# Performance work log

Measured on AMD Instinct MI355X. Metric: run time of the kernel, lower is better.

## Reference

```python
import jax, jax.numpy as jnp
import numpy as np

L, D, FF, H, S, B, W = 4, 768, 3072, 12, 4096, 4, 128


def setup_inputs() -> dict:
    key = jax.random.key(0)
    ks = jax.random.split(key, 8)
    w_ = lambda k, shape: jax.random.normal(k, shape, jnp.float32) * 0.02
    return {
        "x": jax.random.normal(ks[0], (B, S, D), jnp.float32),
        "Wq": w_(ks[1], (L, D, D)), "bq": jnp.zeros((L, D), jnp.float32),
        "Wk": w_(ks[2], (L, D, D)), "bk": jnp.zeros((L, D), jnp.float32),
        "Wv": w_(ks[3], (L, D, D)), "bv": jnp.zeros((L, D), jnp.float32),
        "W1": w_(ks[4], (L, D, FF)), "b1": jnp.zeros((L, FF), jnp.float32),
        "W2": w_(ks[5], (L, FF, D)), "b2": jnp.zeros((L, D), jnp.float32),
        "g1": jnp.ones((L, D), jnp.float32), "beta1": jnp.zeros((L, D), jnp.float32),
        "g2": jnp.ones((L, D), jnp.float32), "beta2": jnp.zeros((L, D), jnp.float32),
        "n_heads": H,
        "window": W,
    }


def _layernorm(x, g, b, eps=1e-5):
    m = jnp.mean(x, axis=-1, keepdims=True)
    v = jnp.mean(jnp.square(x - m), axis=-1, keepdims=True)
    return (x - m) * jax.lax.rsqrt(v + eps) * g + b


def _sliding_attn(x, Wq, bq, Wk, bk, Wv, bv, n_heads, w):
    # Longformer 'sliding_chunks' self-attention, one-sided window w (band 2w+1).
    b_, s_, d_ = x.shape
    hd = d_ // n_heads
    nc = s_ // w  # number of query chunks of size w

    def proj(Wm, bm):
        p = x @ Wm + bm
        return p.reshape(b_, s_, n_heads, hd).transpose(0, 2, 1, 3)  # [B,H,S,hd]

    q = proj(Wq, bq) / jnp.sqrt(jnp.asarray(hd, x.dtype))
    k = proj(Wk, bk)
    v = proj(Wv, bv)

    # pad keys/values by one window each side so every query chunk sees 3w keys
    kp = jnp.pad(k, ((0, 0), (0, 0), (w, w), (0, 0)))
    vp = jnp.pad(v, ((0, 0), (0, 0), (w, w), (0, 0)))
    idx = jnp.arange(nc)[:, None] * w + jnp.arange(3 * w)[None, :]  # [nc, 3w]
    kb = kp[:, :, idx]  # [B,H,nc,3w,hd]
    vb = vp[:, :, idx]
    qc = q.reshape(b_, n_heads, nc, w, hd)

    scores = jnp.einsum('bhcqd,bhckd->bhcqk', qc, kb)  # [B,H,nc,w,3w]

    # band + boundary mask: key pos = c*w + kj - w, query pos = c*w + qi
    c = jnp.arange(nc)[:, None, None]
    qi = jnp.arange(w)[None, :, None]
    kj = jnp.arange(3 * w)[None, None, :]
    rel = kj - qi - w
    kpos = c * w + kj - w
    mask = (jnp.abs(rel) <= w) & (kpos >= 0) & (kpos < s_)  # [nc,w,3w]

    scores = jnp.where(mask[None, None], scores, -jnp.inf)
    attn = jax.nn.softmax(scores, axis=-1)
    out = jnp.einsum('bhcqk,bhckd->bhcqd', attn, vb)  # [B,H,nc,w,hd]
    return out.reshape(b_, n_heads, s_, hd).transpose(0, 2, 1, 3).reshape(b_, s_, d_)


def reference(x, Wq, bq, Wk, bk, Wv, bv, W1, b1, W2, b2, g1, beta1, g2, beta2,
              n_heads, window):
    n_layers = Wq.shape[0]
    for l in range(n_layers):
        attn = _sliding_attn(x, Wq[l], bq[l], Wk[l], bk[l], Wv[l], bv[l],
                             n_heads, window)
        x = _layernorm(x + attn, g1[l], beta1[l])
        h = jnp.maximum(x @ W1[l] + b1[l], 0.0) @ W2[l] + b2[l]
        x = _layernorm(x + h, g2[l], beta2[l])
    return x
```

## Files before the change

kernel.cpp:

```cpp
#include <hip/hip_runtime.h>
#include <hip/hip_bf16.h>
#include <type_traits>

#define LAYERS 4
#define D      768
#define FF     3072
#define NH     12
#define HD     64
#define SEQ    4096
#define BATCH  4
#define WIN    128
#define NC     (SEQ / WIN)
#define NTOK   (BATCH * SEQ)

using bf16 = __hip_bfloat16;
typedef short short8 __attribute__((ext_vector_type(8)));
typedef short short4v __attribute__((ext_vector_type(4)));
typedef float floatx4 __attribute__((ext_vector_type(4)));

__device__ __forceinline__ float b2f(unsigned short u) {
    return __uint_as_float(((unsigned)u) << 16);
}
__device__ __forceinline__ short f2bs(float f) {
    union { bf16 h; short s; } u; u.h = __float2bfloat16(f); return u.s;
}
__device__ __forceinline__ void st_cvt(float* p, float v) { *p = v; }
__device__ __forceinline__ void st_cvt(bf16* p, float v) { *p = __float2bfloat16(v); }

__device__ __forceinline__ void gl_lds16(const void* g, void* l) {
    __builtin_amdgcn_global_load_lds(
        (const __attribute__((address_space(1))) void*)g,
        (__attribute__((address_space(3))) void*)l, 16, 0, 0);
}

#define SB0   __builtin_amdgcn_sched_barrier(0)
#define BAR   __builtin_amdgcn_s_barrier()
#define VM4   asm volatile("s_waitcnt vmcnt(4)" ::: "memory")
#define VM0   asm volatile("s_waitcnt vmcnt(0)" ::: "memory")
#define SP1   __builtin_amdgcn_s_setprio(1)
#define SP0   __builtin_amdgcn_s_setprio(0)

__global__ __launch_bounds__(256)
void cvt_f32_bf16(const float* __restrict__ src, bf16* __restrict__ dst)
{
    const int i = (blockIdx.x * 256 + threadIdx.x) * 8;
    const float4 a0 = *(const float4*)(src + i);
    const float4 a1 = *(const float4*)(src + i + 4);
    short8 p = { f2bs(a0.x), f2bs(a0.y), f2bs(a0.z), f2bs(a0.w),
                 f2bs(a1.x), f2bs(a1.y), f2bs(a1.z), f2bs(a1.w) };
    *(short8*)((short*)dst + i) = p;
}

__global__ __launch_bounds__(256)
void transpose_cvt(const float* __restrict__ src, bf16* __restrict__ dst, int K, int N)
{
    __shared__ float t[32][33];
    const int n0 = blockIdx.x * 32, k0 = blockIdx.y * 32;
    const int tx = threadIdx.x & 31, ty = threadIdx.x >> 5;
    #pragma unroll
    for (int r = 0; r < 4; ++r)
        t[ty + 8 * r][tx] = src[(size_t)(k0 + ty + 8 * r) * N + n0 + tx];
    __syncthreads();
    #pragma unroll
    for (int r = 0; r < 4; ++r)
        dst[(size_t)(n0 + ty + 8 * r) * K + k0 + tx] = __float2bfloat16(t[tx][ty + 8 * r]);
}

template<int OMODE, int RELU>
__global__ __launch_bounds__(512, 2)
void gemm8(const bf16* __restrict__ A, const bf16* __restrict__ Wt,
           const float* __restrict__ b0, const float* __restrict__ b1p,
           const float* __restrict__ b2p, bf16* __restrict__ C,
           int K, int N)
{
    extern __shared__ char ldsc[];
    const int tid  = threadIdx.x;
    const int lane = tid & 63;
    const int wave = tid >> 6;
    const int quad = lane >> 4, l16 = lane & 15;
    const int wm = wave >> 2, wn = wave & 3;

    const int bx  = blockIdx.x;
    const int bxs = (bx & 7) * 8 + (bx >> 3);
    const int row0 = bxs * 256;
    const int col0 = blockIdx.y * 256;

    const int lin0 = wave * 1024 + lane * 16;
    const int lin1 = 8192 + wave * 1024 + lane * 16;
    const int rl0 = lin0 >> 7, rl1 = lin1 >> 7;
    const int so0 = (lin0 & 127) ^ ((rl0 & 7) << 4);
    const int so1 = (lin1 & 127) ^ ((rl1 & 7) << 4);
    const char* agl0 = (const char*)A  + 2 * ((size_t)(row0 + rl0) * K) + so0;
    const char* agl1 = (const char*)A  + 2 * ((size_t)(row0 + rl1) * K) + so1;
    const char* bgl0 = (const char*)Wt + 2 * ((size_t)(col0 + rl0) * K) + so0;
    const char* bgl1 = (const char*)Wt + 2 * ((size_t)(col0 + rl1) * K) + so1;
    const size_t hstr = (size_t)128 * K * 2;

#define STA(d,h,kt) do { \
    gl_lds16(agl0 + ((h) ? hstr : 0) + (size_t)(kt) * 128, ldsc + ((d)*2+(h))*16384 + lin0); \
    gl_lds16(agl1 + ((h) ? hstr : 0) + (size_t)(kt) * 128, ldsc + ((d)*2+(h))*16384 + lin1); } while (0)
#define STB(d,h,kt) do { \
    gl_lds16(bgl0 + ((h) ? hstr : 0) + (size_t)(kt) * 128, ldsc + 65536 + ((d)*2+(h))*16384 + lin0); \
    gl_lds16(bgl1 + ((h) ? hstr : 0) + (size_t)(kt) * 128, ldsc + 65536 + ((d)*2+(h))*16384 + lin1); } while (0)

    const int arow  = wm * 64 + l16;
    const int abase = arow * 128;
    const int sA    = (arow & 7) << 4;
    const int aof0  = (quad * 16) ^ sA;
    const int aof1  = (64 + quad * 16) ^ sA;
    const int brow  = wn * 32 + l16;
    const int bbase = brow * 128;
    const int sB    = (brow & 7) << 4;
    const int bof0  = (quad * 16) ^ sB;
    const int bof1  = (64 + quad * 16) ^ sB;

    short8 af[4][2], bf0[2][2], bf1[2][2];
    floatx4 acc[2][2][4][2];
    const floatx4 zero = {0.f, 0.f, 0.f, 0.f};
    #pragma unroll
    for (int a = 0; a < 2; ++a)
        #pragma unroll
        for (int b = 0; b < 2; ++b)
            #pragma unroll
            for (int m = 0; m < 4; ++m)
                #pragma unroll
                for (int n = 0; n < 2; ++n) acc[a][b][m][n] = zero;

#define LDA(slot) do { const char* ab_ = ldsc + (slot)*16384 + abase; \
    _Pragma("unroll") for (int m_ = 0; m_ < 4; ++m_) { \
        af[m_][0] = *(const short8*)(ab_ + m_*2048 + aof0); \
        af[m_][1] = *(const short8*)(ab_ + m_*2048 + aof1); } } while (0)
#define LDB(slot, BF) do { const char* bb_ = ldsc + 65536 + (slot)*16384 + bbase; \
    _Pragma("unroll") for (int n_ = 0; n_ < 2; ++n_) { \
        BF[n_][0] = *(const short8*)(bb_ + n_*2048 + bof0); \
        BF[n_][1] = *(const short8*)(bb_ + n_*2048 + bof1); } } while (0)
#define MM(mh, nh, BF) do { \
    _Pragma("unroll") for (int m_ = 0; m_ < 4; ++m_) \
    _Pragma("unroll") for (int n_ = 0; n_ < 2; ++n_) { \
        acc[mh][nh][m_][n_] = __builtin_amdgcn_mfma_f32_16x16x32_bf16(af[m_][0], BF[n_][0], acc[mh][nh][m_][n_], 0, 0, 0); \
        acc[mh][nh][m_][n_] = __builtin_amdgcn_mfma_f32_16x16x32_bf16(af[m_][1], BF[n_][1], acc[mh][nh][m_][n_], 0, 0, 0); } } while (0)

    const int nkt   = K >> 6;
    const int niter = K >> 7;

    STA(0,0,0); STB(0,0,0); STA(0,1,0); STB(0,1,0);
    STA(1,0,1); STB(1,0,1);
    VM4; SB0; BAR; SB0;

    for (int i = 0; i < niter; ++i) {
        const int k1 = 2*i + 1;
        const int k2 = (2*i + 2 < nkt) ? 2*i + 2 : nkt - 1;
        const int k3 = (2*i + 3 < nkt) ? 2*i + 3 : nkt - 1;
        LDA(0); LDB(0, bf0); LDB(1, bf1); STA(1,1,k1); STB(1,1,k1);
        SP1; MM(0,0,bf0); MM(0,1,bf1); SP0; SB0; BAR; SB0;
        LDA(1); STA(0,0,k2); STB(0,0,k2);
        SP1; MM(1,0,bf0); MM(1,1,bf1); SP0; VM4; SB0; BAR; SB0;
        LDA(2); LDB(2, bf0); LDB(3, bf1); STA(0,1,k2); STB(0,1,k2);
        SP1; MM(0,0,bf0); MM(0,1,bf1); SP0; SB0; BAR; SB0;
        LDA(3); STA(1,0,k3); STB(1,0,k3);
        SP1; MM(1,0,bf0); MM(1,1,bf1); SP0; VM4; SB0; BAR; SB0;
    }
    VM0;

#undef STA
#undef STB
#undef LDA
#undef LDB
#undef MM

    constexpr size_t QEc = (size_t)BATCH * NH * SEQ * HD;
    int sel = 0;
    const float* bptr = b0;
    float scl = 1.0f;
    int ccb = col0;
    if constexpr (OMODE == 3) {
        sel  = blockIdx.y / 3;
        bptr = (sel == 0) ? b0 : (sel == 1) ? b1p : b2p;
        scl  = (sel == 0) ? 0.125f : 1.0f;
        ccb  = col0 - sel * 768;
    }
    #pragma unroll
    for (int mh = 0; mh < 2; ++mh)
    #pragma unroll
    for (int nh = 0; nh < 2; ++nh)
    #pragma unroll
    for (int n = 0; n < 2; ++n) {
        const int c  = ccb + nh * 128 + wn * 32 + n * 16 + l16;
        const float bvv = bptr[c];
        #pragma unroll
        for (int m = 0; m < 4; ++m) {
            const int rr0 = row0 + mh * 128 + wm * 64 + m * 16 + quad * 4;
            if constexpr (OMODE == 3) {
                if (sel == 2) {
                    short4v pack;
                    #pragma unroll
                    for (int r = 0; r < 4; ++r)
                        pack[r] = f2bs(acc[mh][nh][m][n][r] + bvv);
                    const int b_ = rr0 >> 12, s_ = rr0 & (SEQ - 1);
                    const int h_ = c >> 6, d_ = c & (HD - 1);
                    bf16* Cv = C + 2 * QEc;
                    *(short4v*)&Cv[(((size_t)(b_ * NH + h_)) * HD + d_) * SEQ + s_] = pack;
                } else {
                    bf16* Cq = C + (size_t)sel * QEc;
                    #pragma unroll
                    for (int r = 0; r < 4; ++r) {
                        const float v = (acc[mh][nh][m][n][r] + bvv) * scl;
                        const int rr = rr0 + r;
                        const int b_ = rr >> 12, s_ = rr & (SEQ - 1);
                        const int h_ = c >> 6, d_ = c & (HD - 1);
                        Cq[(((size_t)(b_ * NH + h_)) * SEQ + s_) * HD + d_] = __float2bfloat16(v);
                    }
                }
            } else {
                #pragma unroll
                for (int r = 0; r < 4; ++r) {
                    float v = acc[mh][nh][m][n][r] + bvv;
                    if (RELU) v = fmaxf(v, 0.f);
                    C[(size_t)(rr0 + r) * N + c] = __float2bfloat16(v);
                }
            }
        }
    }
}

template<int RELU, int OMODE>
__global__ __launch_bounds__(256)
void mfma_gemm_bf(const bf16* __restrict__ A, const bf16* __restrict__ Wt,
                  const float* __restrict__ bias, bf16* __restrict__ C,
                  int M, int N, int K, float scale)
{
    __shared__ __align__(16) short As[128 * 32];
    __shared__ __align__(16) short Bs[128 * 32];
    const int tid  = threadIdx.x;
    const int lane = tid & 63;
    const int wave = tid >> 6;
    const int quad = lane >> 4, l16 = lane & 15;
    const int mw = (wave >> 1) * 64, nw = (wave & 1) * 64;
    const int row0 = blockIdx.x * 128;
    const int col0 = blockIdx.y * 128;

    const unsigned short* Ag = (const unsigned short*)A;
    const unsigned short* Bg = (const unsigned short*)Wt;
    const int sr = lane >> 2;
    const int sc = (lane & 3) * 8;

    floatx4 acc[4][4];
    const floatx4 zero = {0.f, 0.f, 0.f, 0.f};
    #pragma unroll
    for (int i = 0; i < 4; ++i)
        #pragma unroll
        for (int j = 0; j < 4; ++j) acc[i][j] = zero;

    const size_t abase = (size_t)row0 * K;
    const size_t bbase = (size_t)col0 * K;

    for (int k0 = 0; k0 < K; k0 += 32) {
        __syncthreads();
        #pragma unroll
        for (int e = 0; e < 2; ++e) {
            const int seg = wave * 2 + e;
            const int r = seg * 16 + sr;
            gl_lds16(Ag + abase + (size_t)r * K + k0 + sc, &As[seg * 512]);
            gl_lds16(Bg + bbase + (size_t)r * K + k0 + sc, &Bs[seg * 512]);
        }
        __syncthreads();
        short8 af[4], bfr[4];
        #pragma unroll
        for (int i = 0; i < 4; ++i)
            af[i] = *(const short8*)&As[(mw + 16 * i + l16) * 32 + quad * 8];
        #pragma unroll
        for (int j = 0; j < 4; ++j)
            bfr[j] = *(const short8*)&Bs[(nw + 16 * j + l16) * 32 + quad * 8];
        #pragma unroll
        for (int i = 0; i < 4; ++i)
            #pragma unroll
            for (int j = 0; j < 4; ++j)
                acc[i][j] = __builtin_amdgcn_mfma_f32_16x16x32_bf16(af[i], bfr[j], acc[i][j], 0, 0, 0);
    }
    #pragma unroll
    for (int j = 0; j < 4; ++j) {
        const int c = col0 + nw + 16 * j + l16;
        const float bv = bias[c];
        #pragma unroll
        for (int i = 0; i < 4; ++i) {
            const int rr0 = row0 + mw + 16 * i + quad * 4;
            if constexpr (OMODE == 2) {
                short4v pack;
                #pragma unroll
                for (int r = 0; r < 4; ++r)
                    pack[r] = f2bs((acc[i][j][r] + bv) * scale);
                const int b_ = rr0 >> 12, s_ = rr0 & (SEQ - 1);
                const int h_ = c >> 6, d_ = c & (HD - 1);
                *(short4v*)&C[(((size_t)(b_ * NH + h_)) * HD + d_) * SEQ + s_] = pack;
            } else {
                #pragma unroll
                for (int r = 0; r < 4; ++r) {
                    float v = acc[i][j][r] + bv;
                    if (RELU) v = fmaxf(v, 0.f);
                    v *= scale;
                    const int rr = rr0 + r;
                    if constexpr (OMODE == 1) {
                        const int b_ = rr >> 12, s_ = rr & (SEQ - 1);
                        const int h_ = c >> 6, d_ = c & (HD - 1);
                        st_cvt(&C[(((size_t)(b_ * NH + h_)) * SEQ + s_) * HD + d_], v);
                    } else {
                        st_cvt(&C[(size_t)rr * N + c], v);
                    }
                }
            }
        }
    }
}

__global__ __launch_bounds__(256, 2)
void attn_mfma_kernel(const bf16* __restrict__ q, const bf16* __restrict__ k,
                      const bf16* __restrict__ v, bf16* __restrict__ out)
{
    __shared__ __align__(16) short Qs[128][72];
    __shared__ __align__(16) short Ks[64][72];
    __shared__ __align__(16) short Vs[64][72];
    __shared__ __align__(16) short Ps[4][32][72];

    const int c = blockIdx.x, h = blockIdx.y, b = blockIdx.z;
    const int tid = threadIdx.x;
    const int wave = tid >> 6, lane = tid & 63;
    const int quad = lane >> 4, l16 = lane & 15;
    const int qbase = wave * 32;

    const unsigned short* qg = (const unsigned short*)q + ((size_t)(b * NH + h)) * SEQ * HD;
    const unsigned short* kg = (const unsigned short*)k + ((size_t)(b * NH + h)) * SEQ * HD;
    const unsigned short* vg = (const unsigned short*)v + ((size_t)(b * NH + h)) * HD * SEQ;

    #pragma unroll
    for (int e = 0; e < 4; ++e) {
        const int idx = tid + e * 256;
        const int row = idx >> 3, d0 = (idx & 7) * 8;
        *(uint4*)&Qs[row][d0] = *(const uint4*)(qg + (size_t)(c * WIN + row) * HD + d0);
    }

    floatx4 O[2][4];
    const floatx4 zero = {0.f, 0.f, 0.f, 0.f};
    float m_i[2][4], l_i[2][4];
    #pragma unroll
    for (int i = 0; i < 2; ++i)
        #pragma unroll
        for (int r = 0; r < 4; ++r) { m_i[i][r] = -1e30f; l_i[i][r] = 0.f; }
    #pragma unroll
    for (int i = 0; i < 2; ++i)
        #pragma unroll
        for (int dj = 0; dj < 4; ++dj) O[i][dj] = zero;

    for (int sl = 0; sl < 6; ++sl) {
        const int s0 = sl * 64;
        const int kpos0 = c * WIN - WIN + s0;
        if (kpos0 < 0 || kpos0 >= SEQ) continue;
        __syncthreads();
        #pragma unroll
        for (int e = 0; e < 2; ++e) {
            const int idx = tid + e * 256;
            const int row = idx >> 3, d0 = (idx & 7) * 8;
            *(uint4*)&Ks[row][d0] = *(const uint4*)(kg + (size_t)(kpos0 + row) * HD + d0);
            *(uint4*)&Vs[row][d0] = *(const uint4*)(vg + (size_t)row * SEQ + kpos0 + d0);
        }
        __syncthreads();
        short8 aq[2][2], bk2[4][2];
        #pragma unroll
        for (int i = 0; i < 2; ++i)
            #pragma unroll
            for (int hh = 0; hh < 2; ++hh)
                aq[i][hh] = *(const short8*)&Qs[qbase + 16 * i + l16][hh * 32 + quad * 8];
        #pragma unroll
        for (int j = 0; j < 4; ++j)
            #pragma unroll
            for (int hh = 0; hh < 2; ++hh)
                bk2[j][hh] = *(const short8*)&Ks[16 * j + l16][hh * 32 + quad * 8];
        floatx4 sc[2][4];
        #pragma unroll
        for (int i = 0; i < 2; ++i)
            #pragma unroll
            for (int j = 0; j < 4; ++j) {
                floatx4 t = __builtin_amdgcn_mfma_f32_16x16x32_bf16(aq[i][0], bk2[j][0], zero, 0, 0, 0);
                sc[i][j]  = __builtin_amdgcn_mfma_f32_16x16x32_bf16(aq[i][1], bk2[j][1], t, 0, 0, 0);
            }
        #pragma unroll
        for (int i = 0; i < 2; ++i) {
            #pragma unroll
            for (int r = 0; r < 4; ++r) {
                const int qq = qbase + 16 * i + quad * 4 + r;
                float sv[4];
                float mx = -1e30f;
                #pragma unroll
                for (int j = 0; j < 4; ++j) {
                    const int kj = s0 + 16 * j + l16;
                    const bool ok = (kj >= qq) && (kj <= qq + 2 * WIN);
                    const float s = ok ? sc[i][j][r] : -1e30f;
                    sv[j] = s;
                    mx = fmaxf(mx, s);
                }
                mx = fmaxf(mx, __shfl_xor(mx, 1));
                mx = fmaxf(mx, __shfl_xor(mx, 2));
                mx = fmaxf(mx, __shfl_xor(mx, 4));
                mx = fmaxf(mx, __shfl_xor(mx, 8));
                const float mn = fmaxf(m_i[i][r], mx);
                const float corr = __expf(m_i[i][r] - mn);
                m_i[i][r] = mn;
                float ps = 0.f;
                #pragma unroll
                for (int j = 0; j < 4; ++j) {
                    const float p = (sv[j] > -0.9e30f) ? __expf(sv[j] - mn) : 0.f;
                    ps += p;
                    Ps[wave][16 * i + quad * 4 + r][16 * j + l16] = f2bs(p);
                }
                ps += __shfl_xor(ps, 1);
                ps += __shfl_xor(ps, 2);
                ps += __shfl_xor(ps, 4);
                ps += __shfl_xor(ps, 8);
                l_i[i][r] = l_i[i][r] * corr + ps;
                #pragma unroll
                for (int dj = 0; dj < 4; ++dj) O[i][dj][r] *= corr;
            }
        }
        short8 ap[2][2], bv2[4][2];
        #pragma unroll
        for (int i = 0; i < 2; ++i)
            #pragma unroll
            for (int hh = 0; hh < 2; ++hh)
                ap[i][hh] = *(const short8*)&Ps[wave][16 * i + l16][hh * 32 + quad * 8];
        #pragma unroll
        for (int dj = 0; dj < 4; ++dj)
            #pragma unroll
            for (int hh = 0; hh < 2; ++hh)
                bv2[dj][hh] = *(const short8*)&Vs[16 * dj + l16][hh * 32 + quad * 8];
        #pragma unroll
        for (int i = 0; i < 2; ++i)
            #pragma unroll
            for (int dj = 0; dj < 4; ++dj) {
                O[i][dj] = __builtin_amdgcn_mfma_f32_16x16x32_bf16(ap[i][0], bv2[dj][0], O[i][dj], 0, 0, 0);
                O[i][dj] = __builtin_amdgcn_mfma_f32_16x16x32_bf16(ap[i][1], bv2[dj][1], O[i][dj], 0, 0, 0);
            }
    }
    bf16* og = out + ((size_t)b * SEQ + c * WIN) * D + h * HD;
    #pragma unroll
    for (int i = 0; i < 2; ++i) {
        #pragma unroll
        for (int r = 0; r < 4; ++r) {
            const float inv = 1.f / l_i[i][r];
            const int qq = qbase + 16 * i + quad * 4 + r;
            #pragma unroll
            for (int dj = 0; dj < 4; ++dj)
                og[(size_t)qq * D + 16 * dj + l16] = __float2bfloat16(O[i][dj][r] * inv);
        }
    }
}

template<int WBF>
__global__ __launch_bounds__(256)
void add_ln_kernel(const float* __restrict__ xin, const bf16* __restrict__ h,
                   float* __restrict__ xout, bf16* __restrict__ xbf,
                   const float* __restrict__ g, const float* __restrict__ beta)
{
    const int row  = blockIdx.x * 4 + (threadIdx.x >> 6);
    const int lane = threadIdx.x & 63;
    const float* xr = xin + (size_t)row * D;
    const unsigned short* hr = (const unsigned short*)h + (size_t)row * D;
    float t[12];
    float s = 0.f, s2 = 0.f;
    #pragma unroll
    for (int e = 0; e < 3; ++e) {
        const int i = lane * 4 + e * 256;
        const float4  xv = *(const float4*)(xr + i);
        const short4v hv = *(const short4v*)(hr + i);
        #pragma unroll
        for (int j = 0; j < 4; ++j) {
            const float tv = ((const float*)&xv)[j] + b2f(((const unsigned short*)&hv)[j]);
            t[e * 4 + j] = tv; s += tv; s2 += tv * tv;
        }
    }
    #pragma unroll
    for (int off = 1; off < 64; off <<= 1) {
        s  += __shfl_xor(s, off);
        s2 += __shfl_xor(s2, off);
    }
    const float mean = s * (1.f / D);
    const float inv  = rsqrtf(s2 * (1.f / D) - mean * mean + 1e-5f);
    #pragma unroll
    for (int e = 0; e < 3; ++e) {
        const int i = lane * 4 + e * 256;
        const float4 gv = *(const float4*)(g + i);
        const float4 bv = *(const float4*)(beta + i);
        float4 ov; short4v pb;
        #pragma unroll
        for (int j = 0; j < 4; ++j) {
            const float val = (t[e * 4 + j] - mean) * inv * ((const float*)&gv)[j]
                              + ((const float*)&bv)[j];
            ((float*)&ov)[j] = val;
            pb[j] = f2bs(val);
        }
        *(float4*)(xout + (size_t)row * D + i) = ov;
        if constexpr (WBF)
            *(short4v*)((short*)xbf + (size_t)row * D + i) = pb;
    }
}

static void transpose_layer(const float* Wq, const float* Wk, const float* Wv,
                            const float* W1, const float* W2, int l,
                            bf16* wtl, hipStream_t stream)
{
    const size_t DDm = (size_t)D * D, DFFm = (size_t)D * FF;
    transpose_cvt<<<dim3(D / 32, D / 32), 256, 0, stream>>>(
        Wq + (size_t)l * DDm, wtl, D, D);
    transpose_cvt<<<dim3(D / 32, D / 32), 256, 0, stream>>>(
        Wk + (size_t)l * DDm, wtl + DDm, D, D);
    transpose_cvt<<<dim3(D / 32, D / 32), 256, 0, stream>>>(
        Wv + (size_t)l * DDm, wtl + 2 * DDm, D, D);
    transpose_cvt<<<dim3(FF / 32, D / 32), 256, 0, stream>>>(
        W1 + (size_t)l * DFFm, wtl + 3 * DDm, D, FF);
    transpose_cvt<<<dim3(D / 32, FF / 32), 256, 0, stream>>>(
        W2 + (size_t)l * DFFm, wtl + 3 * DDm + DFFm, FF, D);
}

static void run_fast8(const float* x0,
                      const float* Wq, const float* bq, const float* Wk, const float* bk,
                      const float* Wv, const float* bv, const float* W1, const float* b1,
                      const float* W2, const float* b2, const float* g1, const float* be1,
                      const float* g2, const float* be2, float* out,
                      bf16* qb, bf16* kb, bf16* vb, bf16* hb, bf16* mid, bf16* h2,
                      bf16* wt, bf16* xbf, bool hoisted, hipStream_t stream)
{
    const dim3 gQKV(64, 9);
    const dim3 gF1(64, 12);
    const dim3 gF2(64, 3);
    const dim3 ga(NC, NH, BATCH);
    const size_t DDm = (size_t)D * D, DFFm = (size_t)D * FF;
    const size_t LW = 3 * DDm + 2 * DFFm;
    const int SMEM = 131072;

    cvt_f32_bf16<<<NTOK * D / 2048, 256, 0, stream>>>(x0, xbf);
    if (hoisted)
        for (int l = 0; l < LAYERS; ++l)
            transpose_layer(Wq, Wk, Wv, W1, W2, l, wt + (size_t)l * LW, stream);

    for (int l = 0; l < LAYERS; ++l) {
        const float* xin = (l == 0) ? x0 : out;
        bf16* wtl = hoisted ? wt + (size_t)l * LW : wt;
        if (!hoisted)
            transpose_layer(Wq, Wk, Wv, W1, W2, l, wtl, stream);

        gemm8<3, 0><<<gQKV, 512, SMEM, stream>>>(
            xbf, wtl, bq + (size_t)l * D, bk + (size_t)l * D, bv + (size_t)l * D,
            qb, D, 2304);
        attn_mfma_kernel<<<ga, 256, 0, stream>>>(qb, kb, vb, hb);
        add_ln_kernel<1><<<NTOK / 4, 256, 0, stream>>>(xin, hb, out, xbf,
            g1 + (size_t)l * D, be1 + (size_t)l * D);
        gemm8<0, 1><<<gF1, 512, SMEM, stream>>>(
            xbf, wtl + 3 * DDm, b1 + (size_t)l * FF, nullptr, nullptr,
            mid, D, FF);
        gemm8<0, 0><<<gF2, 512, SMEM, stream>>>(
            mid, wtl + 3 * DDm + DFFm, b2 + (size_t)l * D, nullptr, nullptr,
            h2, FF, D);
        add_ln_kernel<1><<<NTOK / 4, 256, 0, stream>>>(out, h2, out, xbf,
            g2 + (size_t)l * D, be2 + (size_t)l * D);
    }
}

static void run_fast_old(const float* x0,
                         const float* Wq, const float* bq, const float* Wk, const float* bk,
                         const float* Wv, const float* bv, const float* W1, const float* b1,
                         const float* W2, const float* b2, const float* g1, const float* be1,
                         const float* g2, const float* be2, float* out,
                         bf16* qb, bf16* kb, bf16* vb, bf16* hb, bf16* mid, bf16* h2,
                         bf16* wt, bf16* xbf, hipStream_t stream)
{
    const dim3 gD(NTOK / 128, D / 128);
    const dim3 gF(NTOK / 128, FF / 128);
    const dim3 ga(NC, NH, BATCH);
    const size_t DDm = (size_t)D * D, DFFm = (size_t)D * FF;

    cvt_f32_bf16<<<NTOK * D / 2048, 256, 0, stream>>>(x0, xbf);
    for (int l = 0; l < LAYERS; ++l) {
        const float* xin = (l == 0) ? x0 : out;
        transpose_layer(Wq, Wk, Wv, W1, W2, l, wt, stream);

        mfma_gemm_bf<0, 1><<<gD, 256, 0, stream>>>(
            xbf, wt, bq + (size_t)l * D, qb, NTOK, D, D, 0.125f);
        mfma_gemm_bf<0, 1><<<gD, 256, 0, stream>>>(
            xbf, wt + DDm, bk + (size_t)l * D, kb, NTOK, D, D, 1.0f);
        mfma_gemm_bf<0, 2><<<gD, 256, 0, stream>>>(
            xbf, wt + 2 * DDm, bv + (size_t)l * D, vb, NTOK, D, D, 1.0f);
        attn_mfma_kernel<<<ga, 256, 0, stream>>>(qb, kb, vb, hb);
        add_ln_kernel<1><<<NTOK / 4, 256, 0, stream>>>(xin, hb, out, xbf,
            g1 + (size_t)l * D, be1 + (size_t)l * D);
        mfma_gemm_bf<1, 0><<<gF, 256, 0, stream>>>(
            xbf, wt + 3 * DDm, b1 + (size_t)l * FF, mid, NTOK, FF, D, 1.0f);
        mfma_gemm_bf<0, 0><<<gD, 256, 0, stream>>>(
            mid, wt + 3 * DDm + DFFm, b2 + (size_t)l * D, h2, NTOK, D, FF, 1.0f);
        add_ln_kernel<1><<<NTOK / 4, 256, 0, stream>>>(out, h2, out, xbf,
            g2 + (size_t)l * D, be2 + (size_t)l * D);
    }
}

extern "C" void kernel_launch(void* const* d_in, const int* in_sizes, int n_in,
                              void* d_out, int out_size, void* d_ws, size_t ws_size,
                              hipStream_t stream)
{
    const float* x0  = (const float*)d_in[0];
    const float* Wq  = (const float*)d_in[1];
    const float* bq  = (const float*)d_in[2];
    const float* Wk  = (const float*)d_in[3];
    const float* bk  = (const float*)d_in[4];
    const float* Wv  = (const float*)d_in[5];
    const float* bv  = (const float*)d_in[6];
    const float* W1  = (const float*)d_in[7];
    const float* b1  = (const float*)d_in[8];
    const float* W2  = (const float*)d_in[9];
    const float* b2  = (const float*)d_in[10];
    const float* g1  = (const float*)d_in[11];
    const float* be1 = (const float*)d_in[12];
    const float* g2  = (const float*)d_in[13];
    const float* be2 = (const float*)d_in[14];
    float* out = (float*)d_out;

    const size_t QE = (size_t)BATCH * NH * SEQ * HD;
    const size_t LW = (size_t)3 * D * D + 2 * (size_t)D * FF;
    bf16* qb  = (bf16*)d_ws;
    bf16* kb  = qb + QE;
    bf16* vb  = kb + QE;
    bf16* hb  = vb + QE;
    bf16* mid = qb;
    bf16* h2  = qb + 4 * QE;
    bf16* wt  = qb + 5 * QE;
    const bool tierA = ws_size >= (6 * QE + (size_t)LAYERS * LW) * sizeof(bf16);
    const bool tierB = ws_size >= (6 * QE + LW) * sizeof(bf16);
    bf16* xbf = wt + (tierA ? (size_t)LAYERS * LW : LW);

    static int attr_state = 0;
    if (attr_state == 0) {
        bool ok = true;
        ok &= hipFuncSetAttribute((const void*)(gemm8<3, 0>),
              hipFuncAttributeMaxDynamicSharedMemorySize, 131072) == hipSuccess;
        ok &= hipFuncSetAttribute((const void*)(gemm8<0, 1>),
              hipFuncAttributeMaxDynamicSharedMemorySize, 131072) == hipSuccess;
        ok &= hipFuncSetAttribute((const void*)(gemm8<0, 0>),
              hipFuncAttributeMaxDynamicSharedMemorySize, 131072) == hipSuccess;
        attr_state = ok ? 1 : -1;
    }

    if (tierB && attr_state == 1) {
        run_fast8(x0, Wq, bq, Wk, bk, Wv, bv, W1, b1, W2, b2, g1, be1, g2, be2,
                  out, qb, kb, vb, hb, mid, h2, wt, xbf, tierA, stream);
    } else if (tierB) {
        run_fast_old(x0, Wq, bq, Wk, bk, Wv, bv, W1, b1, W2, b2, g1, be1, g2, be2,
                     out, qb, kb, vb, hb, mid, h2, wt, xbf, stream);
    }
}
```

Baseline: 1.612 ms.

## Replace 256x256 GEMM with smaller 128x256 tile, static LDS, double buffering

Swaps the large 256x256-tile GEMM, which used 128 KB of dynamic LDS and a four-stage interleaved schedule, for a 128x256 tile with a K-step of 32 and a simple two-buffer pipeline in 48 KB of static LDS. Launch bounds move to 4 blocks per CU and the row grid doubles. The aim is more resident blocks and better latency hiding without the dynamic-LDS attribute setup. In exchange each tile reuses operands less, and every K-step pays a full vmcnt(0) wait plus a barrier. The fallback path now also runs when the workspace is too small.

```diff
diff --git a/kernel.cpp b/kernel.cpp
--- a/kernel.cpp
+++ b/kernel.cpp
@@ -35,7 +35,6 @@
 
 #define SB0   __builtin_amdgcn_sched_barrier(0)
 #define BAR   __builtin_amdgcn_s_barrier()
-#define VM4   asm volatile("s_waitcnt vmcnt(4)" ::: "memory")
 #define VM0   asm volatile("s_waitcnt vmcnt(0)" ::: "memory")
 #define SP1   __builtin_amdgcn_s_setprio(1)
 #define SP0   __builtin_amdgcn_s_setprio(0)
@@ -67,13 +66,13 @@
 }
 
 template<int OMODE, int RELU>
-__global__ __launch_bounds__(512, 2)
-void gemm8(const bf16* __restrict__ A, const bf16* __restrict__ Wt,
+__global__ __launch_bounds__(512, 4)
+void gemm2(const bf16* __restrict__ A, const bf16* __restrict__ Wt,
            const float* __restrict__ b0, const float* __restrict__ b1p,
            const float* __restrict__ b2p, bf16* __restrict__ C,
            int K, int N)
 {
-    extern __shared__ char ldsc[];
+    __shared__ __align__(16) char lds[49152];
     const int tid  = threadIdx.x;
     const int lane = tid & 63;
     const int wave = tid >> 6;
@@ -81,92 +80,70 @@
     const int wm = wave >> 2, wn = wave & 3;
 
     const int bx  = blockIdx.x;
-    const int bxs = (bx & 7) * 8 + (bx >> 3);
-    const int row0 = bxs * 256;
+    const int bxs = (bx & 7) * 16 + (bx >> 3);
+    const int row0 = bxs * 128;
     const int col0 = blockIdx.y * 256;
 
-    const int lin0 = wave * 1024 + lane * 16;
-    const int lin1 = 8192 + wave * 1024 + lane * 16;
-    const int rl0 = lin0 >> 7, rl1 = lin1 >> 7;
-    const int so0 = (lin0 & 127) ^ ((rl0 & 7) << 4);
-    const int so1 = (lin1 & 127) ^ ((rl1 & 7) << 4);
-    const char* agl0 = (const char*)A  + 2 * ((size_t)(row0 + rl0) * K) + so0;
-    const char* agl1 = (const char*)A  + 2 * ((size_t)(row0 + rl1) * K) + so1;
-    const char* bgl0 = (const char*)Wt + 2 * ((size_t)(col0 + rl0) * K) + so0;
-    const char* bgl1 = (const char*)Wt + 2 * ((size_t)(col0 + rl1) * K) + so1;
-    const size_t hstr = (size_t)128 * K * 2;
-
-#define STA(d,h,kt) do { \
-    gl_lds16(agl0 + ((h) ? hstr : 0) + (size_t)(kt) * 128, ldsc + ((d)*2+(h))*16384 + lin0); \
-    gl_lds16(agl1 + ((h) ? hstr : 0) + (size_t)(kt) * 128, ldsc + ((d)*2+(h))*16384 + lin1); } while (0)
-#define STB(d,h,kt) do { \
-    gl_lds16(bgl0 + ((h) ? hstr : 0) + (size_t)(kt) * 128, ldsc + 65536 + ((d)*2+(h))*16384 + lin0); \
-    gl_lds16(bgl1 + ((h) ? hstr : 0) + (size_t)(kt) * 128, ldsc + 65536 + ((d)*2+(h))*16384 + lin1); } while (0)
-
-    const int arow  = wm * 64 + l16;
-    const int abase = arow * 128;
-    const int sA    = (arow & 7) << 4;
-    const int aof0  = (quad * 16) ^ sA;
-    const int aof1  = (64 + quad * 16) ^ sA;
-    const int brow  = wn * 32 + l16;
-    const int bbase = brow * 128;
-    const int sB    = (brow & 7) << 4;
-    const int bof0  = (quad * 16) ^ sB;
-    const int bof1  = (64 + quad * 16) ^ sB;
-
-    short8 af[4][2], bf0[2][2], bf1[2][2];
-    floatx4 acc[2][2][4][2];
+    const int pA  = tid >> 3, tau = tid & 7;
+    const int uA  = (tau - (pA & 7)) & 7;
+    const int rA  = 2 * pA + (uA >> 2);
+    const int cA  = (uA & 3) * 16;
+    const char* asrc  = (const char*)A  + (size_t)(row0 + rA) * K * 2 + cA;
+    const char* bsrc  = (const char*)Wt + (size_t)(col0 + rA) * K * 2 + cA;
+    const size_t bstr = (size_t)128 * K * 2;
+    char* const dstA  = lds + tid * 16;
+    char* const dstB0 = lds + 16384 + tid * 16;
+    char* const dstB1 = dstB0 + 8192;
+
+#define STG(d, kt) do { \
+    gl_lds16(asrc + (size_t)(kt) * 64, dstA  + (d) * 8192); \
+    gl_lds16(bsrc + (size_t)(kt) * 64, dstB0 + (d) * 16384); \
+    gl_lds16(bsrc + bstr + (size_t)(kt) * 64, dstB1 + (d) * 16384); } while (0)
+
+    int offA[4], offB[4];
+    #pragma unroll
+    for (int i = 0; i < 4; ++i) {
+        const int r = wm * 64 + i * 16 + l16;
+        offA[i] = (r >> 1) * 128 + (((((r & 1) << 2) + quad + ((r >> 1) & 7)) & 7) << 4);
+    }
+    #pragma unroll
+    for (int j = 0; j < 4; ++j) {
+        const int r = wn * 64 + j * 16 + l16;
+        offB[j] = (r >> 1) * 128 + (((((r & 1) << 2) + quad + ((r >> 1) & 7)) & 7) << 4);
+    }
+
+    floatx4 acc[4][4];
     const floatx4 zero = {0.f, 0.f, 0.f, 0.f};
     #pragma unroll
-    for (int a = 0; a < 2; ++a)
-        #pragma unroll
-        for (int b = 0; b < 2; ++b)
-            #pragma unroll
-            for (int m = 0; m < 4; ++m)
-                #pragma unroll
-                for (int n = 0; n < 2; ++n) acc[a][b][m][n] = zero;
-
-#define LDA(slot) do { const char* ab_ = ldsc + (slot)*16384 + abase; \
-    _Pragma("unroll") for (int m_ = 0; m_ < 4; ++m_) { \
-        af[m_][0] = *(const short8*)(ab_ + m_*2048 + aof0); \
-        af[m_][1] = *(const short8*)(ab_ + m_*2048 + aof1); } } while (0)
-#define LDB(slot, BF) do { const char* bb_ = ldsc + 65536 + (slot)*16384 + bbase; \
-    _Pragma("unroll") for (int n_ = 0; n_ < 2; ++n_) { \
-        BF[n_][0] = *(const short8*)(bb_ + n_*2048 + bof0); \
-        BF[n_][1] = *(const short8*)(bb_ + n_*2048 + bof1); } } while (0)
-#define MM(mh, nh, BF) do { \
-    _Pragma("unroll") for (int m_ = 0; m_ < 4; ++m_) \
-    _Pragma("unroll") for (int n_ = 0; n_ < 2; ++n_) { \
-        acc[mh][nh][m_][n_] = __builtin_amdgcn_mfma_f32_16x16x32_bf16(af[m_][0], BF[n_][0], acc[mh][nh][m_][n_], 0, 0, 0); \
-        acc[mh][nh][m_][n_] = __builtin_amdgcn_mfma_f32_16x16x32_bf16(af[m_][1], BF[n_][1], acc[mh][nh][m_][n_], 0, 0, 0); } } while (0)
-
-    const int nkt   = K >> 6;
-    const int niter = K >> 7;
-
-    STA(0,0,0); STB(0,0,0); STA(0,1,0); STB(0,1,0);
-    STA(1,0,1); STB(1,0,1);
-    VM4; SB0; BAR; SB0;
-
-    for (int i = 0; i < niter; ++i) {
-        const int k1 = 2*i + 1;
-        const int k2 = (2*i + 2 < nkt) ? 2*i + 2 : nkt - 1;
-        const int k3 = (2*i + 3 < nkt) ? 2*i + 3 : nkt - 1;
-        LDA(0); LDB(0, bf0); LDB(1, bf1); STA(1,1,k1); STB(1,1,k1);
-        SP1; MM(0,0,bf0); MM(0,1,bf1); SP0; SB0; BAR; SB0;
-        LDA(1); STA(0,0,k2); STB(0,0,k2);
-        SP1; MM(1,0,bf0); MM(1,1,bf1); SP0; VM4; SB0; BAR; SB0;
-        LDA(2); LDB(2, bf0); LDB(3, bf1); STA(0,1,k2); STB(0,1,k2);
-        SP1; MM(0,0,bf0); MM(0,1,bf1); SP0; SB0; BAR; SB0;
-        LDA(3); STA(1,0,k3); STB(1,0,k3);
-        SP1; MM(1,0,bf0); MM(1,1,bf1); SP0; VM4; SB0; BAR; SB0;
-    }
-    VM0;
-
-#undef STA
-#undef STB
-#undef LDA
-#undef LDB
-#undef MM
+    for (int i = 0; i < 4; ++i)
+        #pragma unroll
+        for (int j = 0; j < 4; ++j) acc[i][j] = zero;
+
+    const int nk = K >> 5;
+    STG(0, 0);
+    VM0; SB0; BAR; SB0;
+
+    for (int k = 0; k < nk; ++k) {
+        const int cur = k & 1;
+        const int kn  = (k + 1 < nk) ? k + 1 : k;
+        STG(cur ^ 1, kn);
+        const char* ab = lds + cur * 8192;
+        const char* bb = lds + 16384 + cur * 16384;
+        short8 af[4], bfr[4];
+        #pragma unroll
+        for (int i = 0; i < 4; ++i) af[i]  = *(const short8*)(ab + offA[i]);
+        #pragma unroll
+        for (int j = 0; j < 4; ++j) bfr[j] = *(const short8*)(bb + offB[j]);
+        SP1;
+        #pragma unroll
+        for (int i = 0; i < 4; ++i)
+            #pragma unroll
+            for (int j = 0; j < 4; ++j)
+                acc[i][j] = __builtin_amdgcn_mfma_f32_16x16x32_bf16(af[i], bfr[j], acc[i][j], 0, 0, 0);
+        SP0;
+        VM0; SB0; BAR; SB0;
+    }
+#undef STG
 
     constexpr size_t QEc = (size_t)BATCH * NH * SEQ * HD;
     int sel = 0;
@@ -180,22 +157,18 @@
         ccb  = col0 - sel * 768;
     }
     #pragma unroll
-    for (int mh = 0; mh < 2; ++mh)
-    #pragma unroll
-    for (int nh = 0; nh < 2; ++nh)
-    #pragma unroll
-    for (int n = 0; n < 2; ++n) {
-        const int c  = ccb + nh * 128 + wn * 32 + n * 16 + l16;
+    for (int j = 0; j < 4; ++j) {
+        const int c = ccb + wn * 64 + j * 16 + l16;
         const float bvv = bptr[c];
         #pragma unroll
-        for (int m = 0; m < 4; ++m) {
-            const int rr0 = row0 + mh * 128 + wm * 64 + m * 16 + quad * 4;
+        for (int i = 0; i < 4; ++i) {
+            const int rr0 = row0 + wm * 64 + i * 16 + quad * 4;
             if constexpr (OMODE == 3) {
                 if (sel == 2) {
                     short4v pack;
                     #pragma unroll
                     for (int r = 0; r < 4; ++r)
-                        pack[r] = f2bs(acc[mh][nh][m][n][r] + bvv);
+                        pack[r] = f2bs(acc[i][j][r] + bvv);
                     const int b_ = rr0 >> 12, s_ = rr0 & (SEQ - 1);
                     const int h_ = c >> 6, d_ = c & (HD - 1);
                     bf16* Cv = C + 2 * QEc;
@@ -204,7 +177,7 @@
                     bf16* Cq = C + (size_t)sel * QEc;
                     #pragma unroll
                     for (int r = 0; r < 4; ++r) {
-                        const float v = (acc[mh][nh][m][n][r] + bvv) * scl;
+                        const float v = (acc[i][j][r] + bvv) * scl;
                         const int rr = rr0 + r;
                         const int b_ = rr >> 12, s_ = rr & (SEQ - 1);
                         const int h_ = c >> 6, d_ = c & (HD - 1);
@@ -214,7 +187,7 @@
             } else {
                 #pragma unroll
                 for (int r = 0; r < 4; ++r) {
-                    float v = acc[mh][nh][m][n][r] + bvv;
+                    float v = acc[i][j][r] + bvv;
                     if (RELU) v = fmaxf(v, 0.f);
                     C[(size_t)(rr0 + r) * N + c] = __float2bfloat16(v);
                 }
@@ -527,13 +500,12 @@
                       bf16* qb, bf16* kb, bf16* vb, bf16* hb, bf16* mid, bf16* h2,
                       bf16* wt, bf16* xbf, bool hoisted, hipStream_t stream)
 {
-    const dim3 gQKV(64, 9);
-    const dim3 gF1(64, 12);
-    const dim3 gF2(64, 3);
+    const dim3 gQKV(128, 9);
+    const dim3 gF1(128, 12);
+    const dim3 gF2(128, 3);
     const dim3 ga(NC, NH, BATCH);
     const size_t DDm = (size_t)D * D, DFFm = (size_t)D * FF;
     const size_t LW = 3 * DDm + 2 * DFFm;
-    const int SMEM = 131072;
 
     cvt_f32_bf16<<<NTOK * D / 2048, 256, 0, stream>>>(x0, xbf);
     if (hoisted)
@@ -546,16 +518,16 @@
         if (!hoisted)
             transpose_layer(Wq, Wk, Wv, W1, W2, l, wtl, stream);
 
-        gemm8<3, 0><<<gQKV, 512, SMEM, stream>>>(
+        gemm2<3, 0><<<gQKV, 512, 0, stream>>>(
             xbf, wtl, bq + (size_t)l * D, bk + (size_t)l * D, bv + (size_t)l * D,
             qb, D, 2304);
         attn_mfma_kernel<<<ga, 256, 0, stream>>>(qb, kb, vb, hb);
         add_ln_kernel<1><<<NTOK / 4, 256, 0, stream>>>(xin, hb, out, xbf,
             g1 + (size_t)l * D, be1 + (size_t)l * D);
-        gemm8<0, 1><<<gF1, 512, SMEM, stream>>>(
+        gemm2<0, 1><<<gF1, 512, 0, stream>>>(
             xbf, wtl + 3 * DDm, b1 + (size_t)l * FF, nullptr, nullptr,
             mid, D, FF);
-        gemm8<0, 0><<<gF2, 512, SMEM, stream>>>(
+        gemm2<0, 0><<<gF2, 512, 0, stream>>>(
             mid, wtl + 3 * DDm + DFFm, b2 + (size_t)l * D, nullptr, nullptr,
             h2, FF, D);
         add_ln_kernel<1><<<NTOK / 4, 256, 0, stream>>>(out, h2, out, xbf,
@@ -633,22 +605,10 @@
     const bool tierB = ws_size >= (6 * QE + LW) * sizeof(bf16);
     bf16* xbf = wt + (tierA ? (size_t)LAYERS * LW : LW);
 
-    static int attr_state = 0;
-    if (attr_state == 0) {
-        bool ok = true;
-        ok &= hipFuncSetAttribute((const void*)(gemm8<3, 0>),
-              hipFuncAttributeMaxDynamicSharedMemorySize, 131072) == hipSuccess;
-        ok &= hipFuncSetAttribute((const void*)(gemm8<0, 1>),
-              hipFuncAttributeMaxDynamicSharedMemorySize, 131072) == hipSuccess;
-        ok &= hipFuncSetAttribute((const void*)(gemm8<0, 0>),
-              hipFuncAttributeMaxDynamicSharedMemorySize, 131072) == hipSuccess;
-        attr_state = ok ? 1 : -1;
-    }
-
-    if (tierB && attr_state == 1) {
+    if (tierB) {
         run_fast8(x0, Wq, bq, Wk, bk, Wv, bv, W1, b1, W2, b2, g1, be1, g2, be2,
                   out, qb, kb, vb, hb, mid, h2, wt, xbf, tierA, stream);
-    } else if (tierB) {
+    } else {
         run_fast_old(x0, Wq, bq, Wk, bk, Wv, bv, W1, b1, W2, b2, g1, be1, g2, be2,
                      out, qb, kb, vb, hb, mid, h2, wt, xbf, stream);
     }
```

New measurement: 1.886 ms. 17.0% more time.

## Prefetch next K/V slice into registers and stage attention output through LDS

Applied to the files above, without the earlier changes.

The sliding-window attention kernel now computes the valid slice range up front instead of skipping boundary slices inside the loop. It prefetches the next 64-key K/V slice into registers while the current slice is computed, so global loads overlap with MFMA work. The Q fragments are loaded into registers once, outside the loop. Output is written to LDS first and then stored to global memory as coalesced 16-byte vectors instead of scattered 2-byte stores. This costs more registers, adds an extra barrier per slice, and reuses the Q shared buffer for output staging, which assumes its row pitch fits 144 bytes.

```diff
diff --git a/kernel.cpp b/kernel.cpp
--- a/kernel.cpp
+++ b/kernel.cpp
@@ -338,6 +338,29 @@
         *(uint4*)&Qs[row][d0] = *(const uint4*)(qg + (size_t)(c * WIN + row) * HD + d0);
     }
 
+    const int sl0 = (c == 0) ? 2 : 0;
+    const int sl1 = (66 - 2 * c < 6) ? 66 - 2 * c : 6;
+
+    const int srow = tid >> 3, sd0 = (tid & 7) * 8;
+    uint4 kr[2], vr[2];
+    {
+        const int kp = c * WIN - WIN + sl0 * 64;
+        #pragma unroll
+        for (int e = 0; e < 2; ++e) {
+            const int row = srow + e * 32;
+            kr[e] = *(const uint4*)(kg + (size_t)(kp + row) * HD + sd0);
+            vr[e] = *(const uint4*)(vg + (size_t)row * SEQ + kp + sd0);
+        }
+    }
+
+    __syncthreads();
+    short8 aq[2][2];
+    #pragma unroll
+    for (int i = 0; i < 2; ++i)
+        #pragma unroll
+        for (int hh = 0; hh < 2; ++hh)
+            aq[i][hh] = *(const short8*)&Qs[qbase + 16 * i + l16][hh * 32 + quad * 8];
+
     floatx4 O[2][4];
     const floatx4 zero = {0.f, 0.f, 0.f, 0.f};
     float m_i[2][4], l_i[2][4];
@@ -350,25 +373,25 @@
         #pragma unroll
         for (int dj = 0; dj < 4; ++dj) O[i][dj] = zero;
 
-    for (int sl = 0; sl < 6; ++sl) {
+    for (int sl = sl0; sl < sl1; ++sl) {
+        #pragma unroll
+        for (int e = 0; e < 2; ++e) {
+            const int row = srow + e * 32;
+            *(uint4*)&Ks[row][sd0] = kr[e];
+            *(uint4*)&Vs[row][sd0] = vr[e];
+        }
+        __syncthreads();
+        if (sl + 1 < sl1) {
+            const int kp = c * WIN - WIN + (sl + 1) * 64;
+            #pragma unroll
+            for (int e = 0; e < 2; ++e) {
+                const int row = srow + e * 32;
+                kr[e] = *(const uint4*)(kg + (size_t)(kp + row) * HD + sd0);
+                vr[e] = *(const uint4*)(vg + (size_t)row * SEQ + kp + sd0);
+            }
+        }
         const int s0 = sl * 64;
-        const int kpos0 = c * WIN - WIN + s0;
-        if (kpos0 < 0 || kpos0 >= SEQ) continue;
-        __syncthreads();
-        #pragma unroll
-        for (int e = 0; e < 2; ++e) {
-            const int idx = tid + e * 256;
-            const int row = idx >> 3, d0 = (idx & 7) * 8;
-            *(uint4*)&Ks[row][d0] = *(const uint4*)(kg + (size_t)(kpos0 + row) * HD + d0);
-            *(uint4*)&Vs[row][d0] = *(const uint4*)(vg + (size_t)row * SEQ + kpos0 + d0);
-        }
-        __syncthreads();
-        short8 aq[2][2], bk2[4][2];
-        #pragma unroll
-        for (int i = 0; i < 2; ++i)
-            #pragma unroll
-            for (int hh = 0; hh < 2; ++hh)
-                aq[i][hh] = *(const short8*)&Qs[qbase + 16 * i + l16][hh * 32 + quad * 8];
+        short8 bk2[4][2];
         #pragma unroll
         for (int j = 0; j < 4; ++j)
             #pragma unroll
@@ -438,18 +461,30 @@
                 O[i][dj] = __builtin_amdgcn_mfma_f32_16x16x32_bf16(ap[i][0], bv2[dj][0], O[i][dj], 0, 0, 0);
                 O[i][dj] = __builtin_amdgcn_mfma_f32_16x16x32_bf16(ap[i][1], bv2[dj][1], O[i][dj], 0, 0, 0);
             }
-    }
-    bf16* og = out + ((size_t)b * SEQ + c * WIN) * D + h * HD;
+        __syncthreads();
+    }
+
+    char* const ob = (char*)&Qs[0][0];
     #pragma unroll
     for (int i = 0; i < 2; ++i) {
         #pragma unroll
         for (int r = 0; r < 4; ++r) {
             const float inv = 1.f / l_i[i][r];
-            const int qq = qbase + 16 * i + quad * 4 + r;
+            const int row = qbase + 16 * i + quad * 4 + r;
             #pragma unroll
             for (int dj = 0; dj < 4; ++dj)
-                og[(size_t)qq * D + 16 * dj + l16] = __float2bfloat16(O[i][dj][r] * inv);
-        }
+                *(short*)(ob + row * 144 + (16 * dj + l16) * 2) =
+                    f2bs(O[i][dj][r] * inv);
+        }
+    }
+    __syncthreads();
+    {
+        const int row = tid >> 1;
+        const char* src = ob + row * 144 + (tid & 1) * 64;
+        bf16* og = out + ((size_t)b * SEQ + c * WIN + row) * D + h * HD + (tid & 1) * 32;
+        #pragma unroll
+        for (int e = 0; e < 4; ++e)
+            *(uint4*)((char*)og + e * 16) = *(const uint4*)(src + e * 16);
     }
 }
 
```

New measurement: 1.736 ms. 1.08x slower.
